# Kernel optimization log

Measured on AMD Instinct MI355X. Metric: run time of the kernel, lower is better.

## Reference

```python
import jax, jax.numpy as jnp
import numpy as np

H = 16       # num heads
HD = 64      # head dim
D = H * HD   # hidden size

def _rotate_half(x):
    x1, x2 = jnp.split(x, 2, axis=-1)
    return jnp.concatenate([-x2, x1], axis=-1)

def setup_inputs() -> dict:
    key = jax.random.key(0)
    ks = jax.random.split(key, 12)
    B, N, NP = 16, 1029, 1024  # batch, tokens (5 prefix + 1024 patches), patch tokens
    inp = {
        "hidden_states": jax.random.normal(ks[0], (B, N, D), dtype=jnp.float32),
        "sin": jax.random.uniform(ks[1], (NP, HD), dtype=jnp.float32, minval=-1.0, maxval=1.0),
        "cos": jax.random.uniform(ks[2], (NP, HD), dtype=jnp.float32, minval=-1.0, maxval=1.0),
        "Wq": jax.random.normal(ks[3], (D, D), dtype=jnp.float32) * 0.02,
        "bq": jnp.zeros((D,), dtype=jnp.float32),
        "Wk": jax.random.normal(ks[4], (D, D), dtype=jnp.float32) * 0.02,
        "bk": jnp.zeros((D,), dtype=jnp.float32),
        "Wv": jax.random.normal(ks[5], (D, D), dtype=jnp.float32) * 0.02,
        "bv": jnp.zeros((D,), dtype=jnp.float32),
        "Wo": jax.random.normal(ks[6], (D, D), dtype=jnp.float32) * 0.02,
        "bo": jnp.zeros((D,), dtype=jnp.float32),
    }
    return inp

def reference(hidden_states, sin, cos, Wq, bq, Wk, bk, Wv, bv, Wo, bo):
    B, N, _ = hidden_states.shape
    scaling = HD ** -0.5
    # qkv projections (nn.Linear: x @ W.T + b), split to heads: [B,H,N,HD]
    def proj(W, b):
        y = hidden_states @ W.T + b
        return y.reshape(B, N, H, HD).transpose(0, 2, 1, 3)
    q, k, v = proj(Wq, bq), proj(Wk, bk), proj(Wv, bv)
    # rotary pos emb on patch-token suffix only
    prefix = N - sin.shape[-2]
    def rope(x):
        xs = x[:, :, prefix:, :]
        xs = xs * cos + _rotate_half(xs) * sin
        return jnp.concatenate([x[:, :, :prefix, :], xs], axis=2)
    q, k = rope(q), rope(k)
    # eager attention: softmax in fp32
    attn = jnp.einsum("bhqd,bhkd->bhqk", q, k) * scaling
    attn = jax.nn.softmax(attn.astype(jnp.float32), axis=-1).astype(q.dtype)
    out = jnp.einsum("bhqk,bhkd->bhqd", attn, v)
    out = out.transpose(0, 2, 1, 3).reshape(B, N, D)
    return out @ Wo.T + bo
```

## Files before the change

### kernel.cpp

```cpp
#include <hip/hip_runtime.h>
#include <stdint.h>

#define H 16
#define HD 64
#define D 1024
#define NTOK 1029
#define BATCH 16
#define NPAD 1152
#define M_ROWS (BATCH*NTOK)
#define MPAD 16512
#define KB 1024
#define PREFIX 5

typedef unsigned short u16;
typedef __attribute__((ext_vector_type(8))) short short8;
typedef __attribute__((ext_vector_type(4))) short short4v;
typedef __attribute__((ext_vector_type(4))) float float4v;
typedef __attribute__((ext_vector_type(4))) unsigned int uint4v;

__device__ __forceinline__ u16 f2bf(float x) {
  unsigned int u = __float_as_uint(x);
  u += 0x7FFFu + ((u >> 16) & 1u);
  return (u16)(u >> 16);
}

__device__ __forceinline__ void gload16(const void* g, void* l) {
  __builtin_amdgcn_global_load_lds((const __attribute__((address_space(1))) void*)g,
                                   (__attribute__((address_space(3))) void*)l, 16, 0, 0);
}

__global__ __launch_bounds__(256) void cvt_A_kernel(const float* __restrict__ src,
                                                    u16* __restrict__ dst) {
  int idx = blockIdx.x * 256 + threadIdx.x;
  int m = idx >> 8, k = (idx & 255) * 4;
  float4v x = (float4v)0.f;
  if (m < M_ROWS) x = *(const float4v*)(src + (size_t)m * D + k);
  short4v o;
#pragma unroll
  for (int j = 0; j < 4; j++) o[j] = (short)f2bf(x[j]);
  *(short4v*)(dst + (size_t)m * D + k) = o;
}

__global__ __launch_bounds__(256) void cvt_W_kernel(
    const float* __restrict__ w0, const float* __restrict__ w1,
    const float* __restrict__ w2, const float* __restrict__ w3,
    u16* __restrict__ e0, u16* __restrict__ e1, u16* __restrict__ e2, u16* __restrict__ e3) {
  const float* src = (blockIdx.y == 0) ? w0 : (blockIdx.y == 1) ? w1 : (blockIdx.y == 2) ? w2 : w3;
  u16* dst = (blockIdx.y == 0) ? e0 : (blockIdx.y == 1) ? e1 : (blockIdx.y == 2) ? e2 : e3;
  int idx = blockIdx.x * 256 + threadIdx.x;
  int m = idx >> 8, k = (idx & 255) * 4;
  float4v x = *(const float4v*)(src + (size_t)m * D + k);
  short4v o;
#pragma unroll
  for (int j = 0; j < 4; j++) o[j] = (short)f2bf(x[j]);
  *(short4v*)(dst + (size_t)m * D + k) = o;
}

__device__ __forceinline__ void gemm_mainloop(const u16* __restrict__ A,
                                              const u16* __restrict__ Bw,
                                              u16* As, u16* Bs, int mtile, int ntile,
                                              float4v acc[4][4]) {
  const int tid = threadIdx.x;
  const int lane = tid & 63;
  const int wave = tid >> 6;
  const int wm = (wave >> 1) * 64;
  const int wn = (wave & 1) * 64;
  const int ar = lane & 15;
  const int kq = lane >> 4;
#pragma unroll
  for (int i = 0; i < 4; i++)
#pragma unroll
    for (int j = 0; j < 4; j++) acc[i][j] = (float4v)0.f;

  const size_t abase = (size_t)mtile * 128 * KB;
  const size_t bbase = (size_t)ntile * 128 * KB;
  for (int k0 = 0; k0 < KB; k0 += 32) {
    __syncthreads();
#pragma unroll
    for (int i = 0; i < 2; i++) {
      int chunk = i * 256 + tid;
      gload16(A + abase + (size_t)(chunk >> 2) * KB + k0 + (chunk & 3) * 8,
              As + (size_t)(i * 256 + (tid & ~63)) * 8);
      gload16(Bw + bbase + (size_t)(chunk >> 2) * KB + k0 + (chunk & 3) * 8,
              Bs + (size_t)(i * 256 + (tid & ~63)) * 8);
    }
    __syncthreads();
    short8 af[4], bf[4];
#pragma unroll
    for (int ms = 0; ms < 4; ms++)
      af[ms] = *(const short8*)(As + (wm + ms * 16 + ar) * 32 + kq * 8);
#pragma unroll
    for (int ns = 0; ns < 4; ns++)
      bf[ns] = *(const short8*)(Bs + (wn + ns * 16 + ar) * 32 + kq * 8);
#pragma unroll
    for (int ms = 0; ms < 4; ms++)
#pragma unroll
      for (int ns = 0; ns < 4; ns++)
        acc[ms][ns] = __builtin_amdgcn_mfma_f32_16x16x32_bf16(af[ms], bf[ns], acc[ms][ns], 0, 0, 0);
  }
}

__global__ __launch_bounds__(256) void gemm_qkv_kernel(
    const u16* __restrict__ A,
    const u16* __restrict__ Wqb, const u16* __restrict__ Wkb, const u16* __restrict__ Wvb,
    const float* __restrict__ bq, const float* __restrict__ bk, const float* __restrict__ bv,
    const float* __restrict__ sinp, const float* __restrict__ cosp,
    u16* __restrict__ qb, u16* __restrict__ kb, u16* __restrict__ vt) {
  __shared__ __align__(16) u16 As[128 * 32];
  __shared__ __align__(16) u16 Bs[128 * 32];
  const int z = blockIdx.z;
  const u16* Bw = (z == 0) ? Wqb : (z == 1) ? Wkb : Wvb;
  const float* bias = (z == 0) ? bq : (z == 1) ? bk : bv;
  const int ntile = blockIdx.x, mtile = blockIdx.y;
  float4v acc[4][4];
  gemm_mainloop(A, Bw, As, Bs, mtile, ntile, acc);

  const int tid = threadIdx.x, lane = tid & 63, wave = tid >> 6;
  const int wm = (wave >> 1) * 64, wn = (wave & 1) * 64;
  const int ar = lane & 15, kq = lane >> 4;
#pragma unroll
  for (int ms = 0; ms < 4; ms++) {
#pragma unroll
    for (int r = 0; r < 4; r++) {
      int grow = mtile * 128 + wm + ms * 16 + kq * 4 + r;
      if (grow >= M_ROWS) continue;
      int b = grow / NTOK;
      int n = grow - b * NTOK;
      bool dorope = (z != 2) && (n >= PREFIX);
      int pos = n - PREFIX;
#pragma unroll
      for (int ns = 0; ns < 4; ns++) {
        int col = ntile * 128 + wn + ns * 16 + ar;
        int hh = col >> 6, d = col & 63;
        float y = acc[ms][ns][r] + bias[col];
        if (z == 2) {
          vt[((size_t)(b * H + hh) * 64 + d) * NPAD + n] = f2bf(y);
          continue;
        }
        if (dorope) {
          float xp = acc[ms][ns ^ 2][r] + bias[col ^ 32];
          float c = cosp[pos * HD + d], s = sinp[pos * HD + d];
          y = y * c + ((d < 32) ? -xp : xp) * s;
        }
        if (z == 0) y *= 0.125f;
        u16* outp = (z == 0) ? qb : kb;
        outp[((size_t)(b * H + hh) * NPAD + n) * 64 + d] = f2bf(y);
      }
    }
  }
}

#define SSHIFT 3.0f
#define NJT 17
__global__ __launch_bounds__(256) void attn_kernel(const u16* __restrict__ qb,
                                                   const u16* __restrict__ kb,
                                                   const u16* __restrict__ vt,
                                                   u16* __restrict__ ao) {
  __shared__ __align__(16) u16 sQ[128 * 72];
  __shared__ __align__(16) u16 sK[64 * 72];
  __shared__ __align__(16) u16 sV[64 * 72];
  const int tid = threadIdx.x, lane = tid & 63, wave = tid >> 6;
  const int ar = lane & 15, kq = lane >> 4;
  const int qt = blockIdx.x, hh = blockIdx.y, b = blockIdx.z;
  const int bh = b * H + hh;
  const u16* qbase = qb + (size_t)bh * NPAD * 64;
  const u16* kbase = kb + (size_t)bh * NPAD * 64;
  const u16* vbase = vt + (size_t)bh * 64 * NPAD;

#pragma unroll
  for (int i = 0; i < 4; i++) {
    int chunk = i * 256 + tid;
    int row = chunk >> 3, c = chunk & 7;
    *(uint4v*)(sQ + row * 72 + c * 8) =
        *(const uint4v*)(qbase + (size_t)(qt * 128 + row) * 64 + c * 8);
  }
  __syncthreads();
  short8 aq[2][2];
#pragma unroll
  for (int ms = 0; ms < 2; ms++)
#pragma unroll
    for (int ki = 0; ki < 2; ki++)
      aq[ms][ki] = *(const short8*)(sQ + (wave * 32 + ms * 16 + ar) * 72 + ki * 32 + kq * 8);
  u16* sP = sQ + wave * 32 * 72;

  float rs[2][4];
  float4v o_acc[2][4];
#pragma unroll
  for (int ms = 0; ms < 2; ms++)
#pragma unroll
    for (int r = 0; r < 4; r++) rs[ms][r] = 0.f;
#pragma unroll
  for (int ms = 0; ms < 2; ms++)
#pragma unroll
    for (int t = 0; t < 4; t++) o_acc[ms][t] = (float4v)0.f;

  for (int jt = 0; jt < NJT; jt++) {
    __syncthreads();
#pragma unroll
    for (int i = 0; i < 2; i++) {
      int chunk = i * 256 + tid;
      int row = chunk >> 3, c = chunk & 7;
      *(uint4v*)(sK + row * 72 + c * 8) =
          *(const uint4v*)(kbase + (size_t)(jt * 64 + row) * 64 + c * 8);
      *(uint4v*)(sV + row * 72 + c * 8) =
          *(const uint4v*)(vbase + (size_t)row * NPAD + jt * 64 + c * 8);
    }
    __syncthreads();

    float4v s[2][4];
#pragma unroll
    for (int ms = 0; ms < 2; ms++)
#pragma unroll
      for (int t = 0; t < 4; t++) s[ms][t] = (float4v)0.f;
#pragma unroll
    for (int ki = 0; ki < 2; ki++) {
#pragma unroll
      for (int t = 0; t < 4; t++) {
        short8 bk8 = *(const short8*)(sK + (t * 16 + ar) * 72 + ki * 32 + kq * 8);
#pragma unroll
        for (int ms = 0; ms < 2; ms++)
          s[ms][t] = __builtin_amdgcn_mfma_f32_16x16x32_bf16(aq[ms][ki], bk8, s[ms][t], 0, 0, 0);
      }
    }
    if (jt == NJT - 1) {
#pragma unroll
      for (int t = 0; t < 4; t++)
        if ((NJT - 1) * 64 + t * 16 + ar >= NTOK) {
#pragma unroll
          for (int ms = 0; ms < 2; ms++) s[ms][t] = (float4v)(-INFINITY);
        }
    }
    asm volatile("" ::: "memory");
#pragma unroll
    for (int ms = 0; ms < 2; ms++)
#pragma unroll
      for (int t = 0; t < 4; t++)
#pragma unroll
        for (int r = 0; r < 4; r++) {
          float p = __expf(s[ms][t][r] - SSHIFT);
          rs[ms][r] += p;
          sP[(ms * 16 + kq * 4 + r) * 72 + t * 16 + ar] = f2bf(p);
        }
    asm volatile("" ::: "memory");
#pragma unroll
    for (int ki = 0; ki < 2; ki++) {
#pragma unroll
      for (int ms = 0; ms < 2; ms++) {
        short8 ap = *(const short8*)(sP + (ms * 16 + ar) * 72 + ki * 32 + kq * 8);
#pragma unroll
        for (int t = 0; t < 4; t++) {
          short8 bv8 = *(const short8*)(sV + (t * 16 + ar) * 72 + ki * 32 + kq * 8);
          o_acc[ms][t] = __builtin_amdgcn_mfma_f32_16x16x32_bf16(ap, bv8, o_acc[ms][t], 0, 0, 0);
        }
      }
    }
  }
#pragma unroll
  for (int ms = 0; ms < 2; ms++)
#pragma unroll
    for (int r = 0; r < 4; r++) {
      float l = rs[ms][r];
#pragma unroll
      for (int off = 1; off < 16; off <<= 1) l += __shfl_xor(l, off, 64);
      int i = qt * 128 + wave * 32 + ms * 16 + kq * 4 + r;
      if (i >= NTOK) continue;
      float inv = 1.f / l;
      size_t mg = (size_t)b * NTOK + i;
#pragma unroll
      for (int t = 0; t < 4; t++)
        ao[mg * D + hh * 64 + t * 16 + ar] = f2bf(o_acc[ms][t][r] * inv);
    }
}

__global__ __launch_bounds__(256) void gemm_o_kernel(const u16* __restrict__ A,
                                                     const u16* __restrict__ Wob,
                                                     const float* __restrict__ bo,
                                                     float* __restrict__ out) {
  __shared__ __align__(16) u16 As[128 * 32];
  __shared__ __align__(16) u16 Bs[128 * 32];
  const int ntile = blockIdx.x, mtile = blockIdx.y;
  float4v acc[4][4];
  gemm_mainloop(A, Wob, As, Bs, mtile, ntile, acc);
  const int tid = threadIdx.x, lane = tid & 63, wave = tid >> 6;
  const int wm = (wave >> 1) * 64, wn = (wave & 1) * 64;
  const int ar = lane & 15, kq = lane >> 4;
#pragma unroll
  for (int ms = 0; ms < 4; ms++)
#pragma unroll
    for (int r = 0; r < 4; r++) {
      int grow = mtile * 128 + wm + ms * 16 + kq * 4 + r;
      if (grow >= M_ROWS) continue;
#pragma unroll
      for (int ns = 0; ns < 4; ns++) {
        int col = ntile * 128 + wn + ns * 16 + ar;
        out[(size_t)grow * D + col] = acc[ms][ns][r] + bo[col];
      }
    }
}

extern "C" void kernel_launch(void* const* d_in, const int* in_sizes, int n_in,
                              void* d_out, int out_size, void* d_ws, size_t ws_size,
                              hipStream_t stream) {
  const float* hidden = (const float*)d_in[0];
  const float* sinp = (const float*)d_in[1];
  const float* cosp = (const float*)d_in[2];
  const float* Wq = (const float*)d_in[3]; const float* bq = (const float*)d_in[4];
  const float* Wk = (const float*)d_in[5]; const float* bk = (const float*)d_in[6];
  const float* Wv = (const float*)d_in[7]; const float* bv = (const float*)d_in[8];
  const float* Wo = (const float*)d_in[9]; const float* bo = (const float*)d_in[10];
  float* out = (float*)d_out;
  (void)in_sizes; (void)n_in; (void)out_size; (void)ws_size;

  char* ws = (char*)d_ws;
  size_t off = 0;
  auto carve = [&](size_t elems) {
    u16* p = (u16*)(ws + off);
    off += ((elems * 2 + 255) & ~(size_t)255);
    return p;
  };
  u16* A_bf = carve((size_t)MPAD * KB);
  u16* Wqb = carve((size_t)D * KB);
  u16* Wkb = carve((size_t)D * KB);
  u16* Wvb = carve((size_t)D * KB);
  u16* Wob = carve((size_t)D * KB);
  u16* q_b = carve((size_t)BATCH * H * NPAD * 64);
  u16* k_b = carve((size_t)BATCH * H * NPAD * 64);
  u16* v_t = carve((size_t)BATCH * H * NPAD * 64);

  hipLaunchKernelGGL(cvt_A_kernel, dim3(MPAD), dim3(256), 0, stream, hidden, A_bf);
  hipLaunchKernelGGL(cvt_W_kernel, dim3(1024, 4), dim3(256), 0, stream,
                     Wq, Wk, Wv, Wo, Wqb, Wkb, Wvb, Wob);
  hipLaunchKernelGGL(gemm_qkv_kernel, dim3(8, 129, 3), dim3(256), 0, stream,
                     A_bf, Wqb, Wkb, Wvb, bq, bk, bv, sinp, cosp, q_b, k_b, v_t);
  hipLaunchKernelGGL(attn_kernel, dim3(9, H, BATCH), dim3(256), 0, stream, q_b, k_b, v_t, A_bf);
  hipLaunchKernelGGL(gemm_o_kernel, dim3(8, 129), dim3(256), 0, stream, A_bf, Wob, bo, out);
}
```

Measured before the change: 618.5 us.

## Double K-step per barrier and remap GEMM blocks for XCD-local L2 reuse

The GEMM mainloop now stages a 64-wide K slice (two 32-wide halves) per iteration, halving the number of block-wide barriers and load/compute phase switches. The QKV and output-projection launches use a flat 1D grid whose block index is permuted so that blocks scheduled round-robin onto the same XCD work on nearby tiles. This is intended to improve L2 hit rates for shared A and W tiles. Shared memory per block doubles, which may reduce occupancy.

```diff
diff --git a/kernel.cpp b/kernel.cpp
--- a/kernel.cpp
+++ b/kernel.cpp
@@ -58,7 +58,8 @@
 
 __device__ __forceinline__ void gemm_mainloop(const u16* __restrict__ A,
                                               const u16* __restrict__ Bw,
-                                              u16* As, u16* Bs, int mtile, int ntile,
+                                              u16* As, u16* Bs,
+                                              int mtile, int ntile,
                                               float4v acc[4][4]) {
   const int tid = threadIdx.x;
   const int lane = tid & 63;
@@ -74,29 +75,35 @@
 
   const size_t abase = (size_t)mtile * 128 * KB;
   const size_t bbase = (size_t)ntile * 128 * KB;
-  for (int k0 = 0; k0 < KB; k0 += 32) {
+  for (int k0 = 0; k0 < KB; k0 += 64) {
     __syncthreads();
 #pragma unroll
-    for (int i = 0; i < 2; i++) {
-      int chunk = i * 256 + tid;
-      gload16(A + abase + (size_t)(chunk >> 2) * KB + k0 + (chunk & 3) * 8,
-              As + (size_t)(i * 256 + (tid & ~63)) * 8);
-      gload16(Bw + bbase + (size_t)(chunk >> 2) * KB + k0 + (chunk & 3) * 8,
-              Bs + (size_t)(i * 256 + (tid & ~63)) * 8);
+    for (int h = 0; h < 2; h++) {
+#pragma unroll
+      for (int i = 0; i < 2; i++) {
+        int chunk = i * 256 + tid;
+        gload16(A + abase + (size_t)(chunk >> 2) * KB + k0 + h * 32 + (chunk & 3) * 8,
+                As + h * 4096 + (size_t)(i * 256 + (tid & ~63)) * 8);
+        gload16(Bw + bbase + (size_t)(chunk >> 2) * KB + k0 + h * 32 + (chunk & 3) * 8,
+                Bs + h * 4096 + (size_t)(i * 256 + (tid & ~63)) * 8);
+      }
     }
     __syncthreads();
-    short8 af[4], bf[4];
-#pragma unroll
-    for (int ms = 0; ms < 4; ms++)
-      af[ms] = *(const short8*)(As + (wm + ms * 16 + ar) * 32 + kq * 8);
-#pragma unroll
-    for (int ns = 0; ns < 4; ns++)
-      bf[ns] = *(const short8*)(Bs + (wn + ns * 16 + ar) * 32 + kq * 8);
-#pragma unroll
-    for (int ms = 0; ms < 4; ms++)
+#pragma unroll
+    for (int h = 0; h < 2; h++) {
+      short8 af[4], bf[4];
+#pragma unroll
+      for (int ms = 0; ms < 4; ms++)
+        af[ms] = *(const short8*)(As + h * 4096 + (wm + ms * 16 + ar) * 32 + kq * 8);
 #pragma unroll
       for (int ns = 0; ns < 4; ns++)
-        acc[ms][ns] = __builtin_amdgcn_mfma_f32_16x16x32_bf16(af[ms], bf[ns], acc[ms][ns], 0, 0, 0);
+        bf[ns] = *(const short8*)(Bs + h * 4096 + (wn + ns * 16 + ar) * 32 + kq * 8);
+#pragma unroll
+      for (int ms = 0; ms < 4; ms++)
+#pragma unroll
+        for (int ns = 0; ns < 4; ns++)
+          acc[ms][ns] = __builtin_amdgcn_mfma_f32_16x16x32_bf16(af[ms], bf[ns], acc[ms][ns], 0, 0, 0);
+    }
   }
 }
 
@@ -106,12 +113,15 @@
     const float* __restrict__ bq, const float* __restrict__ bk, const float* __restrict__ bv,
     const float* __restrict__ sinp, const float* __restrict__ cosp,
     u16* __restrict__ qb, u16* __restrict__ kb, u16* __restrict__ vt) {
-  __shared__ __align__(16) u16 As[128 * 32];
-  __shared__ __align__(16) u16 Bs[128 * 32];
-  const int z = blockIdx.z;
+  __shared__ __align__(16) u16 As[2 * 128 * 32];
+  __shared__ __align__(16) u16 Bs[2 * 128 * 32];
+  int L = blockIdx.x;
+  int t = (L & 7) * 387 + (L >> 3);
+  int z = t / 1032;
+  int r = t - z * 1032;
+  const int mtile = r >> 3, ntile = r & 7;
   const u16* Bw = (z == 0) ? Wqb : (z == 1) ? Wkb : Wvb;
   const float* bias = (z == 0) ? bq : (z == 1) ? bk : bv;
-  const int ntile = blockIdx.x, mtile = blockIdx.y;
   float4v acc[4][4];
   gemm_mainloop(A, Bw, As, Bs, mtile, ntile, acc);
 
@@ -121,8 +131,8 @@
 #pragma unroll
   for (int ms = 0; ms < 4; ms++) {
 #pragma unroll
-    for (int r = 0; r < 4; r++) {
-      int grow = mtile * 128 + wm + ms * 16 + kq * 4 + r;
+    for (int r2 = 0; r2 < 4; r2++) {
+      int grow = mtile * 128 + wm + ms * 16 + kq * 4 + r2;
       if (grow >= M_ROWS) continue;
       int b = grow / NTOK;
       int n = grow - b * NTOK;
@@ -132,13 +142,13 @@
       for (int ns = 0; ns < 4; ns++) {
         int col = ntile * 128 + wn + ns * 16 + ar;
         int hh = col >> 6, d = col & 63;
-        float y = acc[ms][ns][r] + bias[col];
+        float y = acc[ms][ns][r2] + bias[col];
         if (z == 2) {
           vt[((size_t)(b * H + hh) * 64 + d) * NPAD + n] = f2bf(y);
           continue;
         }
         if (dorope) {
-          float xp = acc[ms][ns ^ 2][r] + bias[col ^ 32];
+          float xp = acc[ms][ns ^ 2][r2] + bias[col ^ 32];
           float c = cosp[pos * HD + d], s = sinp[pos * HD + d];
           y = y * c + ((d < 32) ? -xp : xp) * s;
         }
@@ -276,9 +286,11 @@
                                                      const u16* __restrict__ Wob,
                                                      const float* __restrict__ bo,
                                                      float* __restrict__ out) {
-  __shared__ __align__(16) u16 As[128 * 32];
-  __shared__ __align__(16) u16 Bs[128 * 32];
-  const int ntile = blockIdx.x, mtile = blockIdx.y;
+  __shared__ __align__(16) u16 As[2 * 128 * 32];
+  __shared__ __align__(16) u16 Bs[2 * 128 * 32];
+  int L = blockIdx.x;
+  int t = (L & 7) * 129 + (L >> 3);
+  const int mtile = t >> 3, ntile = t & 7;
   float4v acc[4][4];
   gemm_mainloop(A, Wob, As, Bs, mtile, ntile, acc);
   const int tid = threadIdx.x, lane = tid & 63, wave = tid >> 6;
@@ -330,8 +342,8 @@
   hipLaunchKernelGGL(cvt_A_kernel, dim3(MPAD), dim3(256), 0, stream, hidden, A_bf);
   hipLaunchKernelGGL(cvt_W_kernel, dim3(1024, 4), dim3(256), 0, stream,
                      Wq, Wk, Wv, Wo, Wqb, Wkb, Wvb, Wob);
-  hipLaunchKernelGGL(gemm_qkv_kernel, dim3(8, 129, 3), dim3(256), 0, stream,
+  hipLaunchKernelGGL(gemm_qkv_kernel, dim3(3096), dim3(256), 0, stream,
                      A_bf, Wqb, Wkb, Wvb, bq, bk, bv, sinp, cosp, q_b, k_b, v_t);
   hipLaunchKernelGGL(attn_kernel, dim3(9, H, BATCH), dim3(256), 0, stream, q_b, k_b, v_t, A_bf);
-  hipLaunchKernelGGL(gemm_o_kernel, dim3(8, 129), dim3(256), 0, stream, A_bf, Wob, bo, out);
-}
+  hipLaunchKernelGGL(gemm_o_kernel, dim3(1032), dim3(256), 0, stream, A_bf, Wob, bo, out);
+}
```

New measurement: 621.1 us. About the same (+0.4%).
